# Optimization experiments

Hardware: AMD Instinct MI355X
Metric: run time of the kernel (lower is better)

## Reference

```python
import jax, jax.numpy as jnp
import numpy as np
import math

B, S, D = 4, 128, 2560
H, HD = 32, 80
FFN = 10240
DEC, ENC = 256, 256
EPS = 1e-5


def setup_inputs() -> dict:
    key = jax.random.key(0)
    ks = iter(jax.random.split(key, 40))

    def w(shape, scale=0.02):
        return jax.random.normal(next(ks), shape, jnp.float32) * scale

    inp = {}
    inp["x"] = jax.random.normal(next(ks), (B, S, D), jnp.float32)
    inp["xa"] = jax.random.normal(next(ks), (B, S, D), jnp.float32)
    # self-attn mask: causal over the S prefill positions, False on unfilled cache tail
    j = jnp.arange(DEC)
    i = jnp.arange(S)
    m = (j[None, :] <= i[:, None]) & (j[None, :] < S)  # [S, DEC]
    inp["mask"] = jnp.broadcast_to(m[None, None], (B, 1, S, DEC))
    inp["cross_mask"] = jnp.broadcast_to((jnp.arange(ENC) < S)[None, None, None], (B, 1, 1, ENC))
    # LayerNorms
    for n in ["ln1", "ln2", "ln3"]:
        inp[n + "_g"] = jnp.ones((D,), jnp.float32)
        inp[n + "_b"] = jnp.zeros((D,), jnp.float32)
    # self-attn projections ([in, out] layout for x @ W)
    for p in ["sa", "ca"]:
        for n in ["wq", "wk", "wv", "wo"]:
            inp[p + "_" + n] = w((D, D))
        for n in ["bq", "bk", "bv", "bo"]:
            inp[p + "_" + n] = jnp.zeros((D,), jnp.float32)
    inp["cache_sk"] = jnp.zeros((B, H, DEC, HD), jnp.float32)
    inp["cache_sv"] = jnp.zeros((B, H, DEC, HD), jnp.float32)
    inp["cache_ck"] = jnp.zeros((B, H, ENC, HD), jnp.float32)
    inp["cache_cv"] = jnp.zeros((B, H, ENC, HD), jnp.float32)
    inp["fc1_w"] = w((D, FFN))
    inp["fc1_b"] = jnp.zeros((FFN,), jnp.float32)
    inp["fc2_w"] = w((FFN, D))
    inp["fc2_b"] = jnp.zeros((D,), jnp.float32)
    return inp


def _ln(h, g, b):
    h32 = h.astype(jnp.float32)
    mu = h32.mean(-1, keepdims=True)
    var = ((h32 - mu) ** 2).mean(-1, keepdims=True)
    return ((h32 - mu) * jax.lax.rsqrt(var + EPS) * g + b).astype(h.dtype)


def _heads(t):
    b, s, _ = t.shape
    return t.reshape(b, s, H, HD).transpose(0, 2, 1, 3)  # [B,H,S,HD]


def _attn(q, k_cache, v_cache, mask):
    kf = k_cache.astype(q.dtype)
    vf = v_cache.astype(q.dtype)
    scores = jnp.einsum("bhqd,bhkd->bhqk", q, kf) / math.sqrt(HD)
    if mask is not None:
        scores = jnp.where(mask, scores, jnp.finfo(scores.dtype).min)
    attn = jax.nn.softmax(scores.astype(jnp.float32), axis=-1).astype(q.dtype)
    o = jnp.einsum("bhqk,bhkd->bhqd", attn, vf)
    b, h, s, hd = o.shape
    return o.transpose(0, 2, 1, 3).reshape(b, s, h * hd)


def reference(x, xa, mask, cross_mask,
              ln1_g, ln1_b, sa_wq, sa_bq, sa_wk, sa_bk, sa_wv, sa_bv, sa_wo, sa_bo,
              cache_sk, cache_sv,
              ln2_g, ln2_b, ca_wq, ca_bq, ca_wk, ca_bk, ca_wv, ca_bv, ca_wo, ca_bo,
              cache_ck, cache_cv,
              ln3_g, ln3_b, fc1_w, fc1_b, fc2_w, fc2_b):
    # --- self-attention (prefill path: scatter with arange indices = prefix write) ---
    h = _ln(x, ln1_g, ln1_b)
    q = _heads(h @ sa_wq + sa_bq)
    k = _heads(h @ sa_wk + sa_bk)
    v = _heads(h @ sa_wv + sa_bv)
    s = q.shape[2]
    sk = cache_sk.at[:, :, :s, :].set(k.astype(jnp.float32))
    sv = cache_sv.at[:, :, :s, :].set(v.astype(jnp.float32))
    o = _attn(q, sk, sv, mask)
    x = x + (o @ sa_wo + sa_bo)

    # --- cross-attention: K/V from encoder output, scattered into cache ---
    h = _ln(x, ln2_g, ln2_b)
    q = _heads(h @ ca_wq + ca_bq)
    k = _heads(xa @ ca_wk + ca_bk)
    v = _heads(xa @ ca_wv + ca_bv)
    kv = k.shape[2]
    ck = cache_ck.at[:, :, :kv, :].set(k.astype(jnp.float32))
    cv = cache_cv.at[:, :, :kv, :].set(v.astype(jnp.float32))
    o = _attn(q, ck, cv, cross_mask)
    x = x + (o @ ca_wo + ca_bo)

    # --- MLP: fc1 -> GELU (exact) -> fc2 ---
    h = _ln(x, ln3_g, ln3_b)
    x = x + (jax.nn.gelu(h @ fc1_w + fc1_b, approximate=False) @ fc2_w + fc2_b)
    return (x, sk, sv, ck, cv)
```

## Files before the change

kernel.cpp:

```cpp
#include <hip/hip_runtime.h>
#include <hip/hip_bf16.h>
#include <math.h>

#define TB   4
#define TS   128
#define TD   2560
#define TH   32
#define THD  80
#define TFFN 10240
#define TDEC 256
#define TM   (TB * TS)
#define CACHE_N ((size_t)TB * TH * TDEC * THD)

using short8  = __attribute__((ext_vector_type(8))) short;
using sshort4 = __attribute__((ext_vector_type(4))) short;
using floatx4 = __attribute__((ext_vector_type(4))) float;

__device__ __forceinline__ short f2bf(float f) {
  unsigned u = __builtin_bit_cast(unsigned, f);
  u += 0x7fff + ((u >> 16) & 1);
  return (short)(u >> 16);
}
__device__ __forceinline__ float bf2f(short s) {
  unsigned u = ((unsigned)(unsigned short)s) << 16;
  return __builtin_bit_cast(float, u);
}

struct GArgs {
  const short* A[3];
  const float* B[3];
  float*       outf[3];
  int tilesPerSeg;
  int nx;
  int N;
  int lda;
  int Kc;
};

__device__ __forceinline__ void stage_load(const short* __restrict__ A,
                                           const float* __restrict__ B,
                                           int lda, int N, int m0, int n0, int k0,
                                           int tid, short8 ra[2], float rb[16])
{
  const int cb = (tid & 3) * 8;
  const int rr = tid >> 2;
#pragma unroll
  for (int it = 0; it < 2; ++it)
    ra[it] = *(const short8*)(A + (size_t)(m0 + rr + it * 64) * lda + k0 + cb);
  const int n  = tid & 127;
  const int kg = (tid >> 7) * 16;
  const float* bp = B + (size_t)(k0 + kg) * N + n0 + n;
#pragma unroll
  for (int j = 0; j < 16; ++j)
    rb[j] = bp[(size_t)j * N];
}

__device__ __forceinline__ void stage_commit(short* __restrict__ As, short* __restrict__ Bs,
                                             int tid, const short8 ra[2], const float rb[16])
{
  const int cb = (tid & 3) * 8;
  const int rr = tid >> 2;
#pragma unroll
  for (int it = 0; it < 2; ++it)
    *(short8*)(&As[(rr + it * 64) * 40 + cb]) = ra[it];
  const int n  = tid & 127;
  const int kg = (tid >> 7) * 16;
  short8 lo, hi;
#pragma unroll
  for (int j = 0; j < 8; ++j) { lo[j] = f2bf(rb[j]); hi[j] = f2bf(rb[8 + j]); }
  *(short8*)(&Bs[n * 40 + kg])     = lo;
  *(short8*)(&Bs[n * 40 + kg + 8]) = hi;
}

__device__ __forceinline__ void compute_step(const short* __restrict__ As,
                                             const short* __restrict__ Bs,
                                             int wm, int wn, int lr, int lq,
                                             floatx4 acc[4][4])
{
  short8 af[4], bfr[4];
#pragma unroll
  for (int t = 0; t < 4; ++t)
    af[t] = *(const short8*)(&As[(wm + t * 16 + lr) * 40 + lq * 8]);
#pragma unroll
  for (int t = 0; t < 4; ++t)
    bfr[t] = *(const short8*)(&Bs[(wn + t * 16 + lr) * 40 + lq * 8]);
#pragma unroll
  for (int tm = 0; tm < 4; ++tm)
#pragma unroll
    for (int tn = 0; tn < 4; ++tn)
      acc[tm][tn] = __builtin_amdgcn_mfma_f32_16x16x32_bf16(af[tm], bfr[tn],
                                                            acc[tm][tn], 0, 0, 0);
}

__global__ __launch_bounds__(256, 3)
void gemmF(GArgs g)
{
  __shared__ short As[128 * 40];
  __shared__ short Bs[128 * 40];

  const int raw = blockIdx.x;
  const int grp = ((raw >> 5) << 3) | (raw & 7);
  const int my  = (raw >> 3) & 3;
  const int z   = grp / g.nx;
  const int x   = grp - z * g.nx;
  const int seg = x / g.tilesPerSeg;
  const int tx  = x - seg * g.tilesPerSeg;

  const short* A = g.A[seg];
  const float* B = g.B[seg];
  const int N = g.N, lda = g.lda;
  const int m0 = my * 128;
  const int n0 = tx * 128;
  const int k0base = z * g.Kc;
  const int nk = g.Kc / 32;

  const int tid = threadIdx.x;
  const int lane = tid & 63;
  const int wv = tid >> 6;
  const int wm = (wv >> 1) * 64;
  const int wn = (wv & 1) * 64;
  const int lr = lane & 15;
  const int lq = lane >> 4;

  floatx4 acc[4][4];
#pragma unroll
  for (int i = 0; i < 4; ++i)
#pragma unroll
    for (int j = 0; j < 4; ++j)
      acc[i][j] = floatx4{0.f, 0.f, 0.f, 0.f};

  short8 raP[2], raF[2];
  float  rbP[16], rbF[16];

  stage_load(A, B, lda, N, m0, n0, k0base, tid, raP, rbP);
  stage_commit(As, Bs, tid, raP, rbP);
  __syncthreads();
  stage_load(A, B, lda, N, m0, n0, k0base + 32, tid, raP, rbP);

  for (int ki = 0; ki < nk; ki += 2) {
    if (ki + 2 < nk)
      stage_load(A, B, lda, N, m0, n0, k0base + (ki + 2) * 32, tid, raF, rbF);
    compute_step(As, Bs, wm, wn, lr, lq, acc);
    __syncthreads();
    stage_commit(As, Bs, tid, raP, rbP);
    __syncthreads();

    if (ki + 3 < nk)
      stage_load(A, B, lda, N, m0, n0, k0base + (ki + 3) * 32, tid, raP, rbP);
    compute_step(As, Bs, wm, wn, lr, lq, acc);
    if (ki + 2 < nk) {
      __syncthreads();
      stage_commit(As, Bs, tid, raF, rbF);
      __syncthreads();
    }
  }

  float* outf = g.outf[seg];
#pragma unroll
  for (int tm = 0; tm < 4; ++tm) {
#pragma unroll
    for (int tn = 0; tn < 4; ++tn) {
      const int col = n0 + wn + tn * 16 + lr;
#pragma unroll
      for (int r = 0; r < 4; ++r) {
        const int row = m0 + wm + tm * 16 + lq * 4 + r;
        outf[(size_t)z * TM * N + (size_t)row * N + col] = acc[tm][tn][r];
      }
    }
  }
}

template<int Z>
__global__ void qkv_combine_kernel(const float* __restrict__ p,
                                   const float* __restrict__ bq,
                                   const float* __restrict__ bk,
                                   const float* __restrict__ bv,
                                   float* __restrict__ qbuf,
                                   float* __restrict__ sk,
                                   float* __restrict__ sv)
{
  const int i4 = blockIdx.x * 256 + threadIdx.x;
  const int row = i4 / 1920;
  const int c4  = i4 - row * 1920;
  const int col = c4 * 4;
  const int seg = (col >= 2 * TD) ? 2 : (col >= TD ? 1 : 0);
  const int c   = col - seg * TD;
  const float* base = p + (size_t)seg * ((size_t)Z * TM * TD) + (size_t)row * TD + c;
  float4 v = *(const float4*)base;
#pragma unroll
  for (int zz = 1; zz < Z; ++zz) {
    float4 t = *(const float4*)(base + (size_t)zz * TM * TD);
    v.x += t.x; v.y += t.y; v.z += t.z; v.w += t.w;
  }
  const float* bias = (seg == 0) ? bq : (seg == 1 ? bk : bv);
  float4 b4 = *(const float4*)(bias + c);
  v.x += b4.x; v.y += b4.y; v.z += b4.z; v.w += b4.w;
  if (seg == 0) {
    *(float4*)(qbuf + (size_t)row * TD + c) = v;
  } else {
    const int hh = c / THD, hd = c % THD;
    const int b = row >> 7, sI = row & 127;
    float* dst = (seg == 1) ? sk : sv;
    *(float4*)(dst + (((size_t)(b * TH + hh) * TDEC + sI) * THD + hd)) = v;
  }
}

template<int Z>
__global__ void fc1_gelu_kernel(const float* __restrict__ p,
                                const float* __restrict__ bias,
                                short* __restrict__ out)
{
  const int i4 = blockIdx.x * 256 + threadIdx.x;
  const int row = i4 / (TFFN / 4);
  const int c4  = i4 - row * (TFFN / 4);
  const int col = c4 * 4;
  const size_t idx = (size_t)row * TFFN + col;
  float4 v = *(const float4*)(p + idx);
#pragma unroll
  for (int zz = 1; zz < Z; ++zz) {
    float4 t = *(const float4*)(p + (size_t)zz * TM * TFFN + idx);
    v.x += t.x; v.y += t.y; v.z += t.z; v.w += t.w;
  }
  float4 b4 = *(const float4*)(bias + col);
  v.x += b4.x; v.y += b4.y; v.z += b4.z; v.w += b4.w;
  sshort4 o;
  o[0] = f2bf(0.5f * v.x * (1.0f + erff(v.x * 0.70710678118654752f)));
  o[1] = f2bf(0.5f * v.y * (1.0f + erff(v.y * 0.70710678118654752f)));
  o[2] = f2bf(0.5f * v.z * (1.0f + erff(v.z * 0.70710678118654752f)));
  o[3] = f2bf(0.5f * v.w * (1.0f + erff(v.w * 0.70710678118654752f)));
  *(sshort4*)(out + idx) = o;
}

template<bool CAUSAL>
__global__ __launch_bounds__(256, 2)
void attn_kernel(const float* __restrict__ q, const float* __restrict__ kc,
                 const float* __restrict__ vc, short* __restrict__ ob)
{
  __shared__ short kb[TS * THD];
  __shared__ short vb[TS * THD];
  __shared__ float qf[64 * 84];
  short* pb = (short*)qf;

  const int tid = threadIdx.x;
  const int bh = blockIdx.x;
  const int b = bh >> 5, h = bh & 31;
  const int r0 = blockIdx.y * 64;

  const size_t cbase = (size_t)bh * TDEC * THD;
  for (int idx = tid; idx < TS * THD; idx += 256) {
    kb[idx] = f2bf(kc[cbase + idx]);
    vb[idx] = f2bf(vc[cbase + idx]);
  }
  for (int idx = tid; idx < 64 * THD; idx += 256) {
    int r = idx / THD, d = idx - r * THD;
    qf[r * 84 + d] = q[(size_t)(b * TS + r0 + r) * TD + h * THD + d];
  }
  __syncthreads();

  const int r = tid >> 2;
  const int quarter = tid & 3;
  const int qi = r0 + r;

  float sc[32];
#pragma unroll 1
  for (int jj = 0; jj < 32; ++jj) {
    int j = quarter + jj * 4;
    if (CAUSAL && j > qi) { sc[jj] = -1e30f; continue; }
    float a = 0.f;
#pragma unroll 8
    for (int d = 0; d < THD; ++d)
      a += qf[r * 84 + d] * bf2f(kb[j * THD + d]);
    sc[jj] = a * 0.11180339887498949f;
  }

  float mx = -1e30f;
#pragma unroll
  for (int jj = 0; jj < 32; ++jj) mx = fmaxf(mx, sc[jj]);
  mx = fmaxf(mx, __shfl_xor(mx, 1));
  mx = fmaxf(mx, __shfl_xor(mx, 2));
  float sum = 0.f;
#pragma unroll
  for (int jj = 0; jj < 32; ++jj) { sc[jj] = __expf(sc[jj] - mx); sum += sc[jj]; }
  sum += __shfl_xor(sum, 1);
  sum += __shfl_xor(sum, 2);
  const float rinv = 1.0f / sum;

  __syncthreads();
#pragma unroll
  for (int jj = 0; jj < 32; ++jj)
    pb[r * TS + quarter + jj * 4] = f2bf(sc[jj] * rinv);
  __syncthreads();

  for (int it = 0; it < 20; ++it) {
    int idx = tid + it * 256;
    int rr = idx / THD, d = idx - rr * THD;
    float a = 0.f;
#pragma unroll 8
    for (int j = 0; j < TS; ++j)
      a += bf2f(pb[rr * TS + j]) * bf2f(vb[j * THD + d]);
    ob[(size_t)(b * TS + r0 + rr) * TD + h * THD + d] = f2bf(a);
  }
}

__global__ __launch_bounds__(256, 4)
void ln_kernel(const float* __restrict__ x, const float* __restrict__ g,
               const float* __restrict__ bb, short* __restrict__ out)
{
  const int row = blockIdx.x;
  const float* xr = x + (size_t)row * TD;
  const int tid = threadIdx.x;
  float vals[10];
  float s = 0.f, ss = 0.f;
#pragma unroll
  for (int it = 0; it < 10; ++it) {
    float v = xr[tid + it * 256];
    vals[it] = v; s += v; ss += v * v;
  }
#pragma unroll
  for (int o = 32; o > 0; o >>= 1) { s += __shfl_xor(s, o); ss += __shfl_xor(ss, o); }
  __shared__ float red[8];
  const int wv = tid >> 6, lane = tid & 63;
  if (lane == 0) { red[wv] = s; red[wv + 4] = ss; }
  __syncthreads();
  s  = red[0] + red[1] + red[2] + red[3];
  ss = red[4] + red[5] + red[6] + red[7];
  const float mu = s * (1.0f / TD);
  const float rstd = rsqrtf(ss * (1.0f / TD) - mu * mu + 1e-5f);
  short* orow = out + (size_t)row * TD;
#pragma unroll
  for (int it = 0; it < 10; ++it) {
    int i = tid + it * 256;
    orow[i] = f2bf((vals[it] - mu) * rstd * g[i] + bb[i]);
  }
}

template<int Z>
__global__ __launch_bounds__(256, 4)
void ln_fuse_kernel(const float* __restrict__ xin, const float* __restrict__ p,
                    const float* __restrict__ obias,
                    const float* __restrict__ g, const float* __restrict__ bb,
                    short* __restrict__ hout, float* __restrict__ xout)
{
  const int row = blockIdx.x;
  const int tid = threadIdx.x;
  const size_t base = (size_t)row * TD;
  float vals[10];
  float s = 0.f, ss = 0.f;
#pragma unroll
  for (int it = 0; it < 10; ++it) {
    int i = tid + it * 256;
    float v = xin[base + i] + obias[i];
#pragma unroll
    for (int zz = 0; zz < Z; ++zz)
      v += p[(size_t)zz * TM * TD + base + i];
    vals[it] = v; xout[base + i] = v; s += v; ss += v * v;
  }
#pragma unroll
  for (int o = 32; o > 0; o >>= 1) { s += __shfl_xor(s, o); ss += __shfl_xor(ss, o); }
  __shared__ float red[8];
  const int wv = tid >> 6, lane = tid & 63;
  if (lane == 0) { red[wv] = s; red[wv + 4] = ss; }
  __syncthreads();
  s  = red[0] + red[1] + red[2] + red[3];
  ss = red[4] + red[5] + red[6] + red[7];
  const float mu = s * (1.0f / TD);
  const float rstd = rsqrtf(ss * (1.0f / TD) - mu * mu + 1e-5f);
#pragma unroll
  for (int it = 0; it < 10; ++it) {
    int i = tid + it * 256;
    hout[base + i] = f2bf((vals[it] - mu) * rstd * g[i] + bb[i]);
  }
}

template<int Z>
__global__ void fc2_combine_kernel(const float* __restrict__ x2, const float* __restrict__ p,
                                   const float* __restrict__ bias, float* __restrict__ out)
{
  const size_t i = ((size_t)blockIdx.x * 256 + threadIdx.x) * 4;
  const int col = (int)(i % TD);
  float4 v = *(const float4*)(x2 + i);
#pragma unroll
  for (int zz = 0; zz < Z; ++zz) {
    float4 t = *(const float4*)(p + (size_t)zz * TM * TD + i);
    v.x += t.x; v.y += t.y; v.z += t.z; v.w += t.w;
  }
  float4 b4 = *(const float4*)(bias + col);
  v.x += b4.x; v.y += b4.y; v.z += b4.z; v.w += b4.w;
  *(float4*)(out + i) = v;
}

__global__ void cvt_bf16_kernel(const float* __restrict__ in, short* __restrict__ out, int n)
{
  int i = blockIdx.x * 256 + threadIdx.x;
  if (i < n) out[i] = f2bf(in[i]);
}

__global__ void tailcopy_kernel(const float* __restrict__ src, float* __restrict__ dst)
{
  int off4 = blockIdx.x * 256 + threadIdx.x;
  int chunk = blockIdx.y;
  size_t pos = (size_t)chunk * 5120 + 2560 + off4;
  ((float4*)dst)[pos] = ((const float4*)src)[pos];
}

extern "C" void kernel_launch(void* const* d_in, const int* in_sizes, int n_in,
                              void* d_out, int out_size, void* d_ws, size_t ws_size,
                              hipStream_t stream)
{
  (void)in_sizes; (void)n_in; (void)out_size; (void)ws_size;
  const float* x        = (const float*)d_in[0];
  const float* xa       = (const float*)d_in[1];
  const float* ln1_g    = (const float*)d_in[4];
  const float* ln1_b    = (const float*)d_in[5];
  const float* ln2_g    = (const float*)d_in[6];
  const float* ln2_b    = (const float*)d_in[7];
  const float* ln3_g    = (const float*)d_in[8];
  const float* ln3_b    = (const float*)d_in[9];
  const float* sa_wq    = (const float*)d_in[10];
  const float* sa_wk    = (const float*)d_in[11];
  const float* sa_wv    = (const float*)d_in[12];
  const float* sa_wo    = (const float*)d_in[13];
  const float* sa_bq    = (const float*)d_in[14];
  const float* sa_bk    = (const float*)d_in[15];
  const float* sa_bv    = (const float*)d_in[16];
  const float* sa_bo    = (const float*)d_in[17];
  const float* ca_wq    = (const float*)d_in[18];
  const float* ca_wk    = (const float*)d_in[19];
  const float* ca_wv    = (const float*)d_in[20];
  const float* ca_wo    = (const float*)d_in[21];
  const float* ca_bq    = (const float*)d_in[22];
  const float* ca_bk    = (const float*)d_in[23];
  const float* ca_bv    = (const float*)d_in[24];
  const float* ca_bo    = (const float*)d_in[25];
  const float* cache_sk = (const float*)d_in[26];
  const float* cache_sv = (const float*)d_in[27];
  const float* cache_ck = (const float*)d_in[28];
  const float* cache_cv = (const float*)d_in[29];
  const float* fc1_w    = (const float*)d_in[30];
  const float* fc1_b    = (const float*)d_in[31];
  const float* fc2_w    = (const float*)d_in[32];
  const float* fc2_b    = (const float*)d_in[33];

  float* out_x  = (float*)d_out;
  float* out_sk = out_x + (size_t)TM * TD;
  float* out_sv = out_sk + CACHE_N;
  float* out_ck = out_sv + CACHE_N;
  float* out_cv = out_ck + CACHE_N;

  char* w = (char*)d_ws;
  short* h_b   = (short*)w; w += (size_t)TM * TD * 2;
  short* xa_b  = (short*)w; w += (size_t)TM * TD * 2;
  short* o_b   = (short*)w; w += (size_t)TM * TD * 2;
  short* ffn_b = (short*)w; w += (size_t)TM * TFFN * 2;
  float* qbuf  = (float*)w; w += (size_t)TM * TD * 4;
  float* x1    = (float*)w; w += (size_t)TM * TD * 4;
  float* x2    = (float*)w; w += (size_t)TM * TD * 4;
  float* pbuf  = (float*)w; w += (size_t)TM * TD * 4 * 12;

  const dim3 blk(256);
  const dim3 gAttn(TB * TH, 2);

  cvt_bf16_kernel<<<dim3(TM * TD / 256), blk, 0, stream>>>(xa, xa_b, TM * TD);
  tailcopy_kernel<<<dim3(10, TB * TH), blk, 0, stream>>>(cache_sk, out_sk);
  tailcopy_kernel<<<dim3(10, TB * TH), blk, 0, stream>>>(cache_sv, out_sv);
  tailcopy_kernel<<<dim3(10, TB * TH), blk, 0, stream>>>(cache_ck, out_ck);
  tailcopy_kernel<<<dim3(10, TB * TH), blk, 0, stream>>>(cache_cv, out_cv);

  ln_kernel<<<dim3(TM), blk, 0, stream>>>(x, ln1_g, ln1_b, h_b);
  {
    GArgs a{};
    a.A[0] = h_b; a.B[0] = sa_wq; a.outf[0] = pbuf;
    a.A[1] = h_b; a.B[1] = sa_wk; a.outf[1] = pbuf + (size_t)4 * TM * TD;
    a.A[2] = h_b; a.B[2] = sa_wv; a.outf[2] = pbuf + (size_t)8 * TM * TD;
    a.tilesPerSeg = 20; a.nx = 60; a.N = TD; a.lda = TD; a.Kc = TD / 4;
    gemmF<<<dim3(960), blk, 0, stream>>>(a);
  }
  qkv_combine_kernel<4><<<dim3(TM * 7680 / 4 / 256), blk, 0, stream>>>(
      pbuf, sa_bq, sa_bk, sa_bv, qbuf, out_sk, out_sv);
  attn_kernel<true><<<gAttn, blk, 0, stream>>>(qbuf, out_sk, out_sv, o_b);
  {
    GArgs a{};
    a.A[0] = o_b; a.B[0] = sa_wo; a.outf[0] = pbuf;
    a.tilesPerSeg = 20; a.nx = 20; a.N = TD; a.lda = TD; a.Kc = TD / 8;
    gemmF<<<dim3(640), blk, 0, stream>>>(a);
  }
  ln_fuse_kernel<8><<<dim3(TM), blk, 0, stream>>>(x, pbuf, sa_bo, ln2_g, ln2_b, h_b, x1);

  {
    GArgs a{};
    a.A[0] = h_b;  a.B[0] = ca_wq; a.outf[0] = pbuf;
    a.A[1] = xa_b; a.B[1] = ca_wk; a.outf[1] = pbuf + (size_t)4 * TM * TD;
    a.A[2] = xa_b; a.B[2] = ca_wv; a.outf[2] = pbuf + (size_t)8 * TM * TD;
    a.tilesPerSeg = 20; a.nx = 60; a.N = TD; a.lda = TD; a.Kc = TD / 4;
    gemmF<<<dim3(960), blk, 0, stream>>>(a);
  }
  qkv_combine_kernel<4><<<dim3(TM * 7680 / 4 / 256), blk, 0, stream>>>(
      pbuf, ca_bq, ca_bk, ca_bv, qbuf, out_ck, out_cv);
  attn_kernel<false><<<gAttn, blk, 0, stream>>>(qbuf, out_ck, out_cv, o_b);
  {
    GArgs a{};
    a.A[0] = o_b; a.B[0] = ca_wo; a.outf[0] = pbuf;
    a.tilesPerSeg = 20; a.nx = 20; a.N = TD; a.lda = TD; a.Kc = TD / 8;
    gemmF<<<dim3(640), blk, 0, stream>>>(a);
  }
  ln_fuse_kernel<8><<<dim3(TM), blk, 0, stream>>>(x1, pbuf, ca_bo, ln3_g, ln3_b, h_b, x2);

  {
    GArgs a{};
    a.A[0] = h_b; a.B[0] = fc1_w; a.outf[0] = pbuf;
    a.tilesPerSeg = 80; a.nx = 80; a.N = TFFN; a.lda = TD; a.Kc = TD / 2;
    gemmF<<<dim3(640), blk, 0, stream>>>(a);
  }
  fc1_gelu_kernel<2><<<dim3(TM * TFFN / 4 / 256), blk, 0, stream>>>(pbuf, fc1_b, ffn_b);
  {
    GArgs a{};
    a.A[0] = ffn_b; a.B[0] = fc2_w; a.outf[0] = pbuf;
    a.tilesPerSeg = 20; a.nx = 20; a.N = TD; a.lda = TFFN; a.Kc = TFFN / 8;
    gemmF<<<dim3(640), blk, 0, stream>>>(a);
  }
  fc2_combine_kernel<8><<<dim3(TM * TD / 4 / 256), blk, 0, stream>>>(x2, pbuf, fc2_b, out_x);
}
```

Baseline: 888.1 us.

## Pre-transpose weights to bf16 K-major layout before GEMMs

Adds a tiled kernel that converts all ten fp32 weight matrices to bf16 and transposes them to an [N][K] layout on every call. The GEMM then loads B with the same vectorized short8 row loads it uses for A, which removes the per-element fp32 strided loads and the in-loop bf16 conversion. This also cuts B register staging from 16 floats to two short8 per stage. In exchange, each call makes an extra full pass that reads all fp32 weights and writes their bf16 copies, and it needs a large extra workspace.

```diff
diff --git a/kernel.cpp b/kernel.cpp
--- a/kernel.cpp
+++ b/kernel.cpp
@@ -26,9 +26,58 @@
   return __builtin_bit_cast(float, u);
 }
 
+struct TArgs {
+  const float* src[10];
+  short*       dst[10];
+  int ntiles[10];
+  int tstart[10];
+};
+
+__global__ __launch_bounds__(256, 8)
+void wtrans_kernel(TArgs t)
+{
+  __shared__ short tile[64][74];
+  const int bid = blockIdx.x;
+  int j = 0;
+#pragma unroll
+  for (int i = 1; i < 10; ++i) if (bid >= t.tstart[i]) j = i;
+  const int rel = bid - t.tstart[j];
+  const int nt  = t.ntiles[j];
+  const int kt  = rel / nt, ntile = rel - kt * nt;
+  const float* src = t.src[j];
+  short* dst = t.dst[j];
+  const int N = nt * 64;
+  const int K = gridDim.x ? 0 : 0;
+  (void)K;
+  const int ktiles = ((j + 1 < 10 ? t.tstart[j + 1] : (int)gridDim.x) - t.tstart[j]) / nt;
+  const int Kdim = ktiles * 64;
+  const int k0 = kt * 64, n0 = ntile * 64;
+  const int tid = threadIdx.x;
+  const int rr = tid >> 4;
+  const int cc = (tid & 15) * 4;
+#pragma unroll
+  for (int it = 0; it < 4; ++it) {
+    const int k = rr + it * 16;
+    float4 v = *(const float4*)(src + (size_t)(k0 + k) * N + n0 + cc);
+    tile[k][cc]     = f2bf(v.x);
+    tile[k][cc + 1] = f2bf(v.y);
+    tile[k][cc + 2] = f2bf(v.z);
+    tile[k][cc + 3] = f2bf(v.w);
+  }
+  __syncthreads();
+#pragma unroll
+  for (int it = 0; it < 4; ++it) {
+    const int n = rr + it * 16;
+    sshort4 o;
+    o[0] = tile[cc][n]; o[1] = tile[cc + 1][n];
+    o[2] = tile[cc + 2][n]; o[3] = tile[cc + 3][n];
+    *(sshort4*)(dst + (size_t)(n0 + n) * Kdim + k0 + cc) = o;
+  }
+}
+
 struct GArgs {
   const short* A[3];
-  const float* B[3];
+  const short* B[3];
   float*       outf[3];
   int tilesPerSeg;
   int nx;
@@ -38,38 +87,29 @@
 };
 
 __device__ __forceinline__ void stage_load(const short* __restrict__ A,
-                                           const float* __restrict__ B,
-                                           int lda, int N, int m0, int n0, int k0,
-                                           int tid, short8 ra[2], float rb[16])
+                                           const short* __restrict__ B,
+                                           int lda, int m0, int n0, int k0,
+                                           int tid, short8 ra[2], short8 rb[2])
 {
   const int cb = (tid & 3) * 8;
   const int rr = tid >> 2;
 #pragma unroll
-  for (int it = 0; it < 2; ++it)
+  for (int it = 0; it < 2; ++it) {
     ra[it] = *(const short8*)(A + (size_t)(m0 + rr + it * 64) * lda + k0 + cb);
-  const int n  = tid & 127;
-  const int kg = (tid >> 7) * 16;
-  const float* bp = B + (size_t)(k0 + kg) * N + n0 + n;
-#pragma unroll
-  for (int j = 0; j < 16; ++j)
-    rb[j] = bp[(size_t)j * N];
+    rb[it] = *(const short8*)(B + (size_t)(n0 + rr + it * 64) * lda + k0 + cb);
+  }
 }
 
 __device__ __forceinline__ void stage_commit(short* __restrict__ As, short* __restrict__ Bs,
-                                             int tid, const short8 ra[2], const float rb[16])
+                                             int tid, const short8 ra[2], const short8 rb[2])
 {
   const int cb = (tid & 3) * 8;
   const int rr = tid >> 2;
 #pragma unroll
-  for (int it = 0; it < 2; ++it)
+  for (int it = 0; it < 2; ++it) {
     *(short8*)(&As[(rr + it * 64) * 40 + cb]) = ra[it];
-  const int n  = tid & 127;
-  const int kg = (tid >> 7) * 16;
-  short8 lo, hi;
-#pragma unroll
-  for (int j = 0; j < 8; ++j) { lo[j] = f2bf(rb[j]); hi[j] = f2bf(rb[8 + j]); }
-  *(short8*)(&Bs[n * 40 + kg])     = lo;
-  *(short8*)(&Bs[n * 40 + kg + 8]) = hi;
+    *(short8*)(&Bs[(rr + it * 64) * 40 + cb]) = rb[it];
+  }
 }
 
 __device__ __forceinline__ void compute_step(const short* __restrict__ As,
@@ -107,7 +147,7 @@
   const int tx  = x - seg * g.tilesPerSeg;
 
   const short* A = g.A[seg];
-  const float* B = g.B[seg];
+  const short* B = g.B[seg];
   const int N = g.N, lda = g.lda;
   const int m0 = my * 128;
   const int n0 = tx * 128;
@@ -129,24 +169,23 @@
     for (int j = 0; j < 4; ++j)
       acc[i][j] = floatx4{0.f, 0.f, 0.f, 0.f};
 
-  short8 raP[2], raF[2];
-  float  rbP[16], rbF[16];
-
-  stage_load(A, B, lda, N, m0, n0, k0base, tid, raP, rbP);
+  short8 raP[2], raF[2], rbP[2], rbF[2];
+
+  stage_load(A, B, lda, m0, n0, k0base, tid, raP, rbP);
   stage_commit(As, Bs, tid, raP, rbP);
   __syncthreads();
-  stage_load(A, B, lda, N, m0, n0, k0base + 32, tid, raP, rbP);
+  stage_load(A, B, lda, m0, n0, k0base + 32, tid, raP, rbP);
 
   for (int ki = 0; ki < nk; ki += 2) {
     if (ki + 2 < nk)
-      stage_load(A, B, lda, N, m0, n0, k0base + (ki + 2) * 32, tid, raF, rbF);
+      stage_load(A, B, lda, m0, n0, k0base + (ki + 2) * 32, tid, raF, rbF);
     compute_step(As, Bs, wm, wn, lr, lq, acc);
     __syncthreads();
     stage_commit(As, Bs, tid, raP, rbP);
     __syncthreads();
 
     if (ki + 3 < nk)
-      stage_load(A, B, lda, N, m0, n0, k0base + (ki + 3) * 32, tid, raP, rbP);
+      stage_load(A, B, lda, m0, n0, k0base + (ki + 3) * 32, tid, raP, rbP);
     compute_step(As, Bs, wm, wn, lr, lq, acc);
     if (ki + 2 < nk) {
       __syncthreads();
@@ -456,9 +495,33 @@
   float* x1    = (float*)w; w += (size_t)TM * TD * 4;
   float* x2    = (float*)w; w += (size_t)TM * TD * 4;
   float* pbuf  = (float*)w; w += (size_t)TM * TD * 4 * 12;
+  short* sa_wqT = (short*)w; w += (size_t)TD * TD * 2;
+  short* sa_wkT = (short*)w; w += (size_t)TD * TD * 2;
+  short* sa_wvT = (short*)w; w += (size_t)TD * TD * 2;
+  short* sa_woT = (short*)w; w += (size_t)TD * TD * 2;
+  short* ca_wqT = (short*)w; w += (size_t)TD * TD * 2;
+  short* ca_wkT = (short*)w; w += (size_t)TD * TD * 2;
+  short* ca_wvT = (short*)w; w += (size_t)TD * TD * 2;
+  short* ca_woT = (short*)w; w += (size_t)TD * TD * 2;
+  short* fc1_wT = (short*)w; w += (size_t)TD * TFFN * 2;
+  short* fc2_wT = (short*)w; w += (size_t)TD * TFFN * 2;
 
   const dim3 blk(256);
   const dim3 gAttn(TB * TH, 2);
+
+  {
+    TArgs t{};
+    const float* s[10] = {sa_wq, sa_wk, sa_wv, sa_wo, ca_wq, ca_wk, ca_wv, ca_wo, fc1_w, fc2_w};
+    short* d[10]       = {sa_wqT, sa_wkT, sa_wvT, sa_woT, ca_wqT, ca_wkT, ca_wvT, ca_woT, fc1_wT, fc2_wT};
+    int nt[10]         = {40, 40, 40, 40, 40, 40, 40, 40, 160, 40};
+    int kt[10]         = {40, 40, 40, 40, 40, 40, 40, 40, 40, 160};
+    int cum = 0;
+    for (int i = 0; i < 10; ++i) {
+      t.src[i] = s[i]; t.dst[i] = d[i]; t.ntiles[i] = nt[i];
+      t.tstart[i] = cum; cum += nt[i] * kt[i];
+    }
+    wtrans_kernel<<<dim3(cum), blk, 0, stream>>>(t);
+  }
 
   cvt_bf16_kernel<<<dim3(TM * TD / 256), blk, 0, stream>>>(xa, xa_b, TM * TD);
   tailcopy_kernel<<<dim3(10, TB * TH), blk, 0, stream>>>(cache_sk, out_sk);
@@ -469,9 +532,9 @@
   ln_kernel<<<dim3(TM), blk, 0, stream>>>(x, ln1_g, ln1_b, h_b);
   {
     GArgs a{};
-    a.A[0] = h_b; a.B[0] = sa_wq; a.outf[0] = pbuf;
-    a.A[1] = h_b; a.B[1] = sa_wk; a.outf[1] = pbuf + (size_t)4 * TM * TD;
-    a.A[2] = h_b; a.B[2] = sa_wv; a.outf[2] = pbuf + (size_t)8 * TM * TD;
+    a.A[0] = h_b; a.B[0] = sa_wqT; a.outf[0] = pbuf;
+    a.A[1] = h_b; a.B[1] = sa_wkT; a.outf[1] = pbuf + (size_t)4 * TM * TD;
+    a.A[2] = h_b; a.B[2] = sa_wvT; a.outf[2] = pbuf + (size_t)8 * TM * TD;
     a.tilesPerSeg = 20; a.nx = 60; a.N = TD; a.lda = TD; a.Kc = TD / 4;
     gemmF<<<dim3(960), blk, 0, stream>>>(a);
   }
@@ -480,7 +543,7 @@
   attn_kernel<true><<<gAttn, blk, 0, stream>>>(qbuf, out_sk, out_sv, o_b);
   {
     GArgs a{};
-    a.A[0] = o_b; a.B[0] = sa_wo; a.outf[0] = pbuf;
+    a.A[0] = o_b; a.B[0] = sa_woT; a.outf[0] = pbuf;
     a.tilesPerSeg = 20; a.nx = 20; a.N = TD; a.lda = TD; a.Kc = TD / 8;
     gemmF<<<dim3(640), blk, 0, stream>>>(a);
   }
@@ -488,9 +551,9 @@
 
   {
     GArgs a{};
-    a.A[0] = h_b;  a.B[0] = ca_wq; a.outf[0] = pbuf;
-    a.A[1] = xa_b; a.B[1] = ca_wk; a.outf[1] = pbuf + (size_t)4 * TM * TD;
-    a.A[2] = xa_b; a.B[2] = ca_wv; a.outf[2] = pbuf + (size_t)8 * TM * TD;
+    a.A[0] = h_b;  a.B[0] = ca_wqT; a.outf[0] = pbuf;
+    a.A[1] = xa_b; a.B[1] = ca_wkT; a.outf[1] = pbuf + (size_t)4 * TM * TD;
+    a.A[2] = xa_b; a.B[2] = ca_wvT; a.outf[2] = pbuf + (size_t)8 * TM * TD;
     a.tilesPerSeg = 20; a.nx = 60; a.N = TD; a.lda = TD; a.Kc = TD / 4;
     gemmF<<<dim3(960), blk, 0, stream>>>(a);
   }
@@ -499,7 +562,7 @@
   attn_kernel<false><<<gAttn, blk, 0, stream>>>(qbuf, out_ck, out_cv, o_b);
   {
     GArgs a{};
-    a.A[0] = o_b; a.B[0] = ca_wo; a.outf[0] = pbuf;
+    a.A[0] = o_b; a.B[0] = ca_woT; a.outf[0] = pbuf;
     a.tilesPerSeg = 20; a.nx = 20; a.N = TD; a.lda = TD; a.Kc = TD / 8;
     gemmF<<<dim3(640), blk, 0, stream>>>(a);
   }
@@ -507,14 +570,14 @@
 
   {
     GArgs a{};
-    a.A[0] = h_b; a.B[0] = fc1_w; a.outf[0] = pbuf;
+    a.A[0] = h_b; a.B[0] = fc1_wT; a.outf[0] = pbuf;
     a.tilesPerSeg = 80; a.nx = 80; a.N = TFFN; a.lda = TD; a.Kc = TD / 2;
     gemmF<<<dim3(640), blk, 0, stream>>>(a);
   }
   fc1_gelu_kernel<2><<<dim3(TM * TFFN / 4 / 256), blk, 0, stream>>>(pbuf, fc1_b, ffn_b);
   {
     GArgs a{};
-    a.A[0] = ffn_b; a.B[0] = fc2_w; a.outf[0] = pbuf;
+    a.A[0] = ffn_b; a.B[0] = fc2_wT; a.outf[0] = pbuf;
     a.tilesPerSeg = 20; a.nx = 20; a.N = TD; a.lda = TFFN; a.Kc = TFFN / 8;
     gemmF<<<dim3(640), blk, 0, stream>>>(a);
   }
```

After: 935.5 us. 1.05x slower.
